# Kernel tuning notes

Hardware: AMD Instinct MI355X
Metric: run time of the kernel (lower is better)

The kernel has to match this reference:

```python
import jax, jax.numpy as jnp
import numpy as np

N_HEAD = 16
N_EMBD = 2048
B, S = 2, 2048


def setup_inputs() -> dict:
    key = jax.random.key(0)
    k1, k2, k3 = jax.random.split(key, 3)
    scale = 0.02
    return {
        "hidden_states": jax.random.normal(k1, (B, S, N_EMBD), dtype=jnp.float32),
        "attention_mask": jnp.ones((B, S), dtype=jnp.float32),
        "w_attn": jax.random.normal(k2, (N_EMBD, 3 * N_EMBD), dtype=jnp.float32) * scale,
        "b_attn": jnp.zeros((3 * N_EMBD,), dtype=jnp.float32),
        "w_proj": jax.random.normal(k3, (N_EMBD, N_EMBD), dtype=jnp.float32) * scale,
        "b_proj": jnp.zeros((N_EMBD,), dtype=jnp.float32),
    }


def reference(hidden_states, attention_mask, w_attn, b_attn, w_proj, b_proj):
    b, s, d = hidden_states.shape
    h = N_HEAD
    dh = d // h
    qkv = hidden_states @ w_attn + b_attn          # [b, s, 3d]
    q, k, v = jnp.split(qkv, 3, axis=-1)
    # [b, s, d] -> [b, h, s, dh]
    q = q.reshape(b, s, h, dh).transpose(0, 2, 1, 3)
    k = k.reshape(b, s, h, dh).transpose(0, 2, 1, 3)
    v = v.reshape(b, s, h, dh).transpose(0, 2, 1, 3)
    scores = jnp.einsum("bhqd,bhkd->bhqk", q, k) / jnp.sqrt(jnp.float32(dh))
    # padding mask: [b, s] -> additive bias [b, 1, 1, s]
    bias = (1.0 - attention_mask)[:, None, None, :] * -10000.0
    attn = jax.nn.softmax(scores + bias, axis=-1)   # dropout p=0 (eval)
    out = jnp.einsum("bhqk,bhkd->bhqd", attn, v)    # [b, h, s, dh]
    out = out.transpose(0, 2, 1, 3).reshape(b, s, d)
    return out @ w_proj + b_proj
```

## Files before the change

kernel.cpp:

```cpp
#include <hip/hip_runtime.h>
#include <stdint.h>

#define B_   2
#define S_   2048
#define D_   2048
#define NH_  16
#define DH_  128
#define N3_  6144

typedef unsigned short u16;
typedef __bf16 bf16x8 __attribute__((ext_vector_type(8)));
typedef float  f32x4  __attribute__((ext_vector_type(4)));

#define QSCALE   (0.08838834764831845f * 1.4426950408889634f)
#define BIASF    (-10000.0f * 1.4426950408889634f)

__device__ __forceinline__ u16 f2bf(float f) {
  union { float f; unsigned u; } v; v.f = f;
  unsigned u = v.u;
  return (u16)((u + 0x7FFFu + ((u >> 16) & 1u)) >> 16);
}

__device__ __forceinline__ float fast_exp2(float x) {
  float r;
  asm("v_exp_f32 %0, %1" : "=v"(r) : "v"(x));
  return r;
}

#define GL2LDS(gsrc, ldst)                                                              \
  __builtin_amdgcn_global_load_lds((const __attribute__((address_space(1))) void*)(gsrc), \
      (__attribute__((address_space(3))) void*)(ldst), 16, 0, 0)

__device__ __forceinline__ int swz_id() {
  int id = blockIdx.y * gridDim.x + blockIdx.x;
  int cpx = (gridDim.x * gridDim.y) >> 3;
  return (id & 7) * cpx + (id >> 3);
}

__global__ void cvt_kernel(const float* __restrict__ in, u16* __restrict__ out, int n4) {
  int i = blockIdx.x * blockDim.x + threadIdx.x;
  int stride = gridDim.x * blockDim.x;
  for (; i < n4; i += stride) {
    float4 v = ((const float4*)in)[i];
    ushort4 o;
    o.x = f2bf(v.x); o.y = f2bf(v.y); o.z = f2bf(v.z); o.w = f2bf(v.w);
    ((ushort4*)out)[i] = o;
  }
}

__global__ void transpose_kernel(const float* __restrict__ in, u16* __restrict__ out,
                                 int K, int N) {
  __shared__ float tile[32][33];
  int tx = threadIdx.x, ty = threadIdx.y;
  int nx = blockIdx.x * 32, ky = blockIdx.y * 32;
#pragma unroll
  for (int j = 0; j < 32; j += 8)
    tile[ty + j][tx] = in[(size_t)(ky + ty + j) * N + nx + tx];
  __syncthreads();
#pragma unroll
  for (int j = 0; j < 32; j += 8)
    out[(size_t)(nx + ty + j) * K + ky + tx] = f2bf(tile[tx][ty + j]);
}


#define KS_ABASE(c, h) (lds + (c) * 24576 + (h) * 8192)
#define KS_BBASE(c, h) (lds + (c) * 24576 + 16384 + (h) * 4096)
#define VMCNT(n) asm volatile("s_waitcnt vmcnt(" #n ")" ::: "memory")
#define LGKM0                                            \
  do {                                                   \
    asm volatile("s_waitcnt lgkmcnt(0)" ::: "memory");   \
    __builtin_amdgcn_sched_barrier(0);                   \
  } while (0)
#define BAR __builtin_amdgcn_s_barrier()

__device__ __forceinline__ void ks_read_set(const u16* __restrict__ Ab,
                                            const u16* __restrict__ Bb,
                                            int wrB, int wcB, int lr, int g,
                                            bf16x8 (&af)[4], bf16x8 (&bf)[4]) {
#pragma unroll
  for (int i = 0; i < 4; ++i) {
    int r = wrB + i * 16 + lr;
    int pr = r >> 1;
    int slot = (((r & 1) << 2) | g) ^ (pr & 7);
    af[i] = *reinterpret_cast<const bf16x8*>(Ab + pr * 64 + slot * 8);
  }
#pragma unroll
  for (int j = 0; j < 4; ++j) {
    int n = wcB + j * 16 + lr;
    int pn = n >> 1;
    int slot = (((n & 1) << 2) | g) ^ (pn & 7);
    bf[j] = *reinterpret_cast<const bf16x8*>(Bb + pn * 64 + slot * 8);
  }
}

__device__ __forceinline__ void ks_mfma(const bf16x8 (&af)[4], const bf16x8 (&bf)[4],
                                        f32x4 (&acc)[4][4]) {
  __builtin_amdgcn_s_setprio(1);
#pragma unroll
  for (int i = 0; i < 4; ++i)
#pragma unroll
    for (int j = 0; j < 4; ++j)
      acc[i][j] = __builtin_amdgcn_mfma_f32_16x16x32_bf16(af[i], bf[j], acc[i][j], 0, 0, 0);
  __builtin_amdgcn_s_setprio(0);
}

template <int KD>
__device__ __forceinline__ void ks_stage(const u16* __restrict__ A,
                                         const u16* __restrict__ BT, u16* lds,
                                         int c, int h, int Tg, int m0, int n0, int t) {
#pragma unroll
  for (int inst = 0; inst < 2; ++inst) {
    int idx = inst * 512 + t;
    int pr = idx >> 3, s = idx & 7, v = s ^ (pr & 7);
    int r = pr * 2 + (v >> 2), g = v & 3;
    GL2LDS(A + (size_t)(m0 + r) * KD + Tg * 64 + h * 32 + g * 8,
           KS_ABASE(c, h) + idx * 8);
  }
  {
    int idx = t;
    int pn = idx >> 3, s = idx & 7, v = s ^ (pn & 7);
    int n = pn * 2 + (v >> 2), g = v & 3;
    GL2LDS(BT + (size_t)(n0 + n) * KD + Tg * 64 + h * 32 + g * 8,
           KS_BBASE(c, h) + idx * 8);
  }
}

template <int KD>
__device__ __forceinline__ void gemm_ks_core(const u16* __restrict__ A,
                                             const u16* __restrict__ BT,
                                             int m0, int n0, u16* lds, f32x4 (&acc)[4][4]) {
  const int NT = KD / 64;
  int t = threadIdx.x, wv = t >> 6, lane = t & 63;
  int g = lane >> 4, lr = lane & 15;
  int wrB = (wv >> 1) * 64, wcB = (wv & 1) * 64;
  bf16x8 af0[4], bf0[4], af1[4], bf1[4];

  ks_stage<KD>(A, BT, lds, 0, 0, 0, m0, n0, t);
  ks_stage<KD>(A, BT, lds, 0, 1, 0, m0, n0, t);
  ks_stage<KD>(A, BT, lds, 1, 0, 1, m0, n0, t);
  ks_stage<KD>(A, BT, lds, 1, 1, 1, m0, n0, t);
  VMCNT(6);
  BAR;
  ks_read_set(KS_ABASE(0, 0), KS_BBASE(0, 0), wrB, wcB, lr, g, af0, bf0);
  LGKM0;
  BAR;

  for (int T = 0; T < NT; ++T) {
    int c = T & 1;
    ks_read_set(KS_ABASE(c, 1), KS_BBASE(c, 1), wrB, wcB, lr, g, af1, bf1);
    if (T + 2 < NT) ks_stage<KD>(A, BT, lds, c, 0, T + 2, m0, n0, t);
    BAR;
    LGKM0;
    ks_mfma(af0, bf0, acc);
    BAR;
    if (T + 2 < NT) {
      VMCNT(3);
      ks_stage<KD>(A, BT, lds, c, 1, T + 2, m0, n0, t);
    } else {
      VMCNT(0);
    }
    BAR;
    if (T + 1 < NT)
      ks_read_set(KS_ABASE(c ^ 1, 0), KS_BBASE(c ^ 1, 0), wrB, wcB, lr, g, af0, bf0);
    LGKM0;
    ks_mfma(af1, bf1, acc);
    BAR;
  }
}

__global__ __launch_bounds__(512, 2) void gemm_qkv_kernel(
    const u16* __restrict__ A, const u16* __restrict__ BT, const float* __restrict__ bias,
    u16* __restrict__ Qb, u16* __restrict__ Kb, u16* __restrict__ VTb) {
  __shared__ __attribute__((aligned(16))) u16 lds[49152];
  f32x4 acc[4][4] = {};
  int sw = swz_id();
  int n0 = (sw % gridDim.x) * 128, m0 = (sw / gridDim.x) * 256;
  gemm_ks_core<2048>(A, BT, m0, n0, lds, acc);
  int t = threadIdx.x, lane = t & 63, wv = t >> 6;
  int g = lane >> 4, lr = lane & 15;
  int wrB = (wv >> 1) * 64, wcB = (wv & 1) * 64;
#pragma unroll
  for (int mi = 0; mi < 4; ++mi) {
    int rowbase = m0 + wrB + mi * 16 + g * 4;
    int b = rowbase >> 11, s = rowbase & 2047;
#pragma unroll
    for (int nj = 0; nj < 4; ++nj) {
      int col = n0 + wcB + nj * 16 + lr;
      float bv = bias[col];
      int sec = col >> 11;
      int within = col & 2047;
      int h = within >> 7, d = within & 127;
      if (sec < 2) {
        float mult = (sec == 0) ? QSCALE : 1.0f;
        u16* dst = (sec == 0 ? Qb : Kb) + ((size_t)(b * NH_ + h) * S_ + s) * DH_ + d;
#pragma unroll
        for (int r = 0; r < 4; ++r) dst[(size_t)r * DH_] = f2bf((acc[mi][nj][r] + bv) * mult);
      } else {
        u16* dst = VTb + ((size_t)(b * NH_ + h) * DH_ + d) * S_ + s;
        ushort4 pk;
        pk.x = f2bf(acc[mi][nj][0] + bv); pk.y = f2bf(acc[mi][nj][1] + bv);
        pk.z = f2bf(acc[mi][nj][2] + bv); pk.w = f2bf(acc[mi][nj][3] + bv);
        *reinterpret_cast<ushort4*>(dst) = pk;
      }
    }
  }
}

__global__ __launch_bounds__(512, 2) void gemm_proj_kernel(
    const u16* __restrict__ A, const u16* __restrict__ BT, const float* __restrict__ bias,
    float* __restrict__ out) {
  __shared__ __attribute__((aligned(16))) u16 lds[49152];
  f32x4 acc[4][4] = {};
  int sw = swz_id();
  int n0 = (sw % gridDim.x) * 128, m0 = (sw / gridDim.x) * 256;
  gemm_ks_core<2048>(A, BT, m0, n0, lds, acc);
  int t = threadIdx.x, lane = t & 63, wv = t >> 6;
  int g = lane >> 4, lr = lane & 15;
  int wrB = (wv >> 1) * 64, wcB = (wv & 1) * 64;
#pragma unroll
  for (int mi = 0; mi < 4; ++mi) {
    int rowbase = m0 + wrB + mi * 16 + g * 4;
#pragma unroll
    for (int nj = 0; nj < 4; ++nj) {
      int col = n0 + wcB + nj * 16 + lr;
      float bv = bias[col];
      float* dst = out + (size_t)rowbase * D_ + col;
#pragma unroll
      for (int r = 0; r < 4; ++r) dst[(size_t)r * D_] = acc[mi][nj][r] + bv;
    }
  }
}

__global__ __launch_bounds__(256) void attn_kernel(
    const u16* __restrict__ Qb, const u16* __restrict__ Kb, const u16* __restrict__ VTb,
    const float* __restrict__ mask, u16* __restrict__ AO) {
  __shared__ __attribute__((aligned(16))) u16 Ks[2][64 * 128];
  __shared__ __attribute__((aligned(16))) u16 Vs[2][128 * 64];
  __shared__ __attribute__((aligned(16))) u16 Ps[4][16 * 64];
  __shared__ float bias_lds[S_];

  int t = threadIdx.x, w = t >> 6, lane = t & 63;
  int g = lane >> 4, lr = lane & 15;
  int sw = swz_id();
  int qt = sw & 31, bh = sw >> 5;
  int b = bh >> 4;
  const u16* Qh = Qb + (size_t)bh * S_ * DH_;
  const u16* Kh = Kb + (size_t)bh * S_ * DH_;
  const u16* Vh = VTb + (size_t)bh * DH_ * S_;
  int q0 = qt * 64 + w * 16;

  for (int i = t; i < S_; i += 256)
    bias_lds[i] = (1.0f - mask[b * S_ + i]) * BIASF;

  bf16x8 aq[4];
#pragma unroll
  for (int kk = 0; kk < 4; ++kk)
    aq[kk] = *reinterpret_cast<const bf16x8*>(Qh + (size_t)(q0 + lr) * DH_ + kk * 32 + g * 8);

  f32x4 oacc[8] = {};
  float m_r[4], l_r[4];
#pragma unroll
  for (int r = 0; r < 4; ++r) { m_r[r] = -1e30f; l_r[r] = 0.f; }

  __syncthreads();

#define STAGE_KV(buf, s0base)                                                    \
  {                                                                              \
    _Pragma("unroll")                                                            \
    for (int i = 0; i < 4; ++i) {                                                \
      int idx = i * 256 + t;                                                     \
      int row = idx >> 4, slot = idx & 15;                                       \
      GL2LDS(Kh + (size_t)((s0base) + row) * DH_ + ((slot ^ (row & 7)) * 8),     \
             &Ks[buf][idx * 8]);                                                 \
    }                                                                            \
    _Pragma("unroll")                                                            \
    for (int i = 0; i < 4; ++i) {                                                \
      int idx = i * 256 + t;                                                     \
      int row = idx >> 3, slot = idx & 7;                                        \
      GL2LDS(Vh + (size_t)row * S_ + (s0base) + ((slot ^ (row & 7)) * 8),        \
             &Vs[buf][idx * 8]);                                                 \
    }                                                                            \
  }

  STAGE_KV(0, 0);
  const int NT = S_ / 64;
  for (int it = 0; it < NT; ++it) {
    int cur = it & 1;
    if (it + 1 < NT) {
      STAGE_KV(cur ^ 1, (it + 1) * 64);
      asm volatile("s_waitcnt vmcnt(8)" ::: "memory");
    } else {
      asm volatile("s_waitcnt vmcnt(0)" ::: "memory");
    }
    __builtin_amdgcn_s_barrier();
    __builtin_amdgcn_sched_barrier(0);

    f32x4 sacc[4] = {};
#pragma unroll
    for (int kk = 0; kk < 4; ++kk) {
#pragma unroll
      for (int n = 0; n < 4; ++n) {
        int c = lr + 16 * n;
        bf16x8 bk = *reinterpret_cast<const bf16x8*>(
            &Ks[cur][c * 128 + ((((kk << 2) | g) ^ (c & 7)) * 8)]);
        sacc[n] = __builtin_amdgcn_mfma_f32_16x16x32_bf16(aq[kk], bk, sacc[n], 0, 0, 0);
      }
    }

    int s0 = it * 64;
    float sv[4][4], mx[4];
#pragma unroll
    for (int r = 0; r < 4; ++r) {
#pragma unroll
      for (int n = 0; n < 4; ++n) sv[r][n] = sacc[n][r] + bias_lds[s0 + lr + 16 * n];
      float m2 = fmaxf(fmaxf(sv[r][0], sv[r][1]), fmaxf(sv[r][2], sv[r][3]));
#pragma unroll
      for (int off = 1; off < 16; off <<= 1) m2 = fmaxf(m2, __shfl_xor(m2, off));
      mx[r] = m2;
    }
    float gmax = fmaxf(fmaxf(mx[0] - m_r[0], mx[1] - m_r[1]),
                       fmaxf(mx[2] - m_r[2], mx[3] - m_r[3]));
    if (__any(gmax > 8.f)) {
#pragma unroll
      for (int r = 0; r < 4; ++r) {
        float mnew = fmaxf(m_r[r], mx[r]);
        float f = fast_exp2(m_r[r] - mnew);
        m_r[r] = mnew;
        l_r[r] *= f;
#pragma unroll
        for (int no = 0; no < 8; ++no) oacc[no][r] *= f;
      }
    }
#pragma unroll
    for (int r = 0; r < 4; ++r) {
      int prow = g * 4 + r;
#pragma unroll
      for (int n = 0; n < 4; ++n) {
        float p = fast_exp2(sv[r][n] - m_r[r]);
        l_r[r] += p;
        int col = lr + 16 * n;
        Ps[w][prow * 64 + ((((col >> 3) ^ (prow & 7)) << 3) + (col & 7))] = f2bf(p);
      }
    }

#pragma unroll
    for (int kk2 = 0; kk2 < 2; ++kk2) {
      bf16x8 ap = *reinterpret_cast<const bf16x8*>(
          &Ps[w][lr * 64 + ((((kk2 << 2) | g) ^ (lr & 7)) * 8)]);
#pragma unroll
      for (int no = 0; no < 8; ++no) {
        int d = lr + 16 * no;
        bf16x8 bv = *reinterpret_cast<const bf16x8*>(
            &Vs[cur][d * 64 + ((((kk2 << 2) | g) ^ (d & 7)) * 8)]);
        oacc[no] = __builtin_amdgcn_mfma_f32_16x16x32_bf16(ap, bv, oacc[no], 0, 0, 0);
      }
    }
    __builtin_amdgcn_sched_barrier(0);
    __builtin_amdgcn_s_barrier();
  }
#undef STAGE_KV

#pragma unroll
  for (int r = 0; r < 4; ++r) {
    float s = l_r[r];
#pragma unroll
    for (int off = 1; off < 16; off <<= 1) s += __shfl_xor(s, off);
    float inv = 1.0f / s;
    int qrow = q0 + g * 4 + r;
    int h = bh & 15;
    u16* dst = AO + ((size_t)(b * S_ + qrow)) * D_ + h * DH_;
#pragma unroll
    for (int no = 0; no < 8; ++no) dst[lr + 16 * no] = f2bf(oacc[no][r] * inv);
  }
}

extern "C" void kernel_launch(void* const* d_in, const int* in_sizes, int n_in,
                              void* d_out, int out_size, void* d_ws, size_t ws_size,
                              hipStream_t stream) {
  const float* h_in   = (const float*)d_in[0];
  const float* mask   = (const float*)d_in[1];
  const float* w_attn = (const float*)d_in[2];
  const float* b_attn = (const float*)d_in[3];
  const float* w_proj = (const float*)d_in[4];
  const float* b_proj = (const float*)d_in[5];
  float* out = (float*)d_out;

  char* ws = (char*)d_ws;
  u16* Hb  = (u16*)(ws);
  u16* W1T = (u16*)(ws + 16777216);
  u16* W2T = (u16*)(ws + 41943040);
  u16* Qb  = (u16*)(ws + 50331648);
  u16* Kb  = (u16*)(ws + 67108864);
  u16* VTb = (u16*)(ws + 83886080);
  u16* AO  = Hb;

  cvt_kernel<<<2048, 256, 0, stream>>>(h_in, Hb, (B_ * S_ * D_) / 4);
  dim3 tb(32, 8);
  transpose_kernel<<<dim3(N3_ / 32, D_ / 32), tb, 0, stream>>>(w_attn, W1T, D_, N3_);
  transpose_kernel<<<dim3(D_ / 32, D_ / 32), tb, 0, stream>>>(w_proj, W2T, D_, D_);
  gemm_qkv_kernel<<<dim3(N3_ / 128, (B_ * S_) / 256), 512, 0, stream>>>(
      Hb, W1T, b_attn, Qb, Kb, VTb);
  attn_kernel<<<dim3(S_ / 64, B_ * NH_), 256, 0, stream>>>(Qb, Kb, VTb, mask, AO);
  gemm_proj_kernel<<<dim3(D_ / 128, (B_ * S_) / 256), 512, 0, stream>>>(AO, W2T, b_proj, out);
}
```

Baseline: 445.3 us.

## Transpose attention MFMAs to keep P in registers and drop LDS round-trip

Swaps the operand order of the QK^T and PV MFMAs so each lane holds one query row's scores. Softmax statistics then need only two cross-lane shuffles, and P is packed with v_cvt_pk_bf16 and redistributed via shuffles instead of being written to and re-read from LDS. The change also adds s_setprio around the MFMA blocks, vectorizes the output and bias accesses, and relaxes the GEMM launch bounds to one block per SIMD. It trades LDS traffic and barriers for extra shuffles and selects, and the GEMM register budget change could alter occupancy.

```diff
diff --git a/kernel.cpp b/kernel.cpp
--- a/kernel.cpp
+++ b/kernel.cpp
@@ -24,6 +24,12 @@
 __device__ __forceinline__ float fast_exp2(float x) {
   float r;
   asm("v_exp_f32 %0, %1" : "=v"(r) : "v"(x));
+  return r;
+}
+
+__device__ __forceinline__ unsigned cvtpk(float lo, float hi) {
+  unsigned r;
+  asm("v_cvt_pk_bf16_f32 %0, %1, %2" : "=v"(r) : "v"(lo), "v"(hi));
   return r;
 }
 
@@ -168,7 +174,7 @@
   }
 }
 
-__global__ __launch_bounds__(512, 2) void gemm_qkv_kernel(
+__global__ __launch_bounds__(512, 1) void gemm_qkv_kernel(
     const u16* __restrict__ A, const u16* __restrict__ BT, const float* __restrict__ bias,
     u16* __restrict__ Qb, u16* __restrict__ Kb, u16* __restrict__ VTb) {
   __shared__ __attribute__((aligned(16))) u16 lds[49152];
@@ -206,7 +212,7 @@
   }
 }
 
-__global__ __launch_bounds__(512, 2) void gemm_proj_kernel(
+__global__ __launch_bounds__(512, 1) void gemm_proj_kernel(
     const u16* __restrict__ A, const u16* __restrict__ BT, const float* __restrict__ bias,
     float* __restrict__ out) {
   __shared__ __attribute__((aligned(16))) u16 lds[49152];
@@ -236,7 +242,6 @@
     const float* __restrict__ mask, u16* __restrict__ AO) {
   __shared__ __attribute__((aligned(16))) u16 Ks[2][64 * 128];
   __shared__ __attribute__((aligned(16))) u16 Vs[2][128 * 64];
-  __shared__ __attribute__((aligned(16))) u16 Ps[4][16 * 64];
   __shared__ float bias_lds[S_];
 
   int t = threadIdx.x, w = t >> 6, lane = t & 63;
@@ -252,15 +257,13 @@
   for (int i = t; i < S_; i += 256)
     bias_lds[i] = (1.0f - mask[b * S_ + i]) * BIASF;
 
-  bf16x8 aq[4];
+  bf16x8 bq[4];
 #pragma unroll
   for (int kk = 0; kk < 4; ++kk)
-    aq[kk] = *reinterpret_cast<const bf16x8*>(Qh + (size_t)(q0 + lr) * DH_ + kk * 32 + g * 8);
+    bq[kk] = *reinterpret_cast<const bf16x8*>(Qh + (size_t)(q0 + lr) * DH_ + kk * 32 + g * 8);
 
   f32x4 oacc[8] = {};
-  float m_r[4], l_r[4];
-#pragma unroll
-  for (int r = 0; r < 4; ++r) { m_r[r] = -1e30f; l_r[r] = 0.f; }
+  float m_r = -1e30f, l_r = 0.f;
 
   __syncthreads();
 
@@ -296,81 +299,91 @@
     __builtin_amdgcn_sched_barrier(0);
 
     f32x4 sacc[4] = {};
+    __builtin_amdgcn_s_setprio(1);
 #pragma unroll
     for (int kk = 0; kk < 4; ++kk) {
 #pragma unroll
       for (int n = 0; n < 4; ++n) {
-        int c = lr + 16 * n;
-        bf16x8 bk = *reinterpret_cast<const bf16x8*>(
-            &Ks[cur][c * 128 + ((((kk << 2) | g) ^ (c & 7)) * 8)]);
-        sacc[n] = __builtin_amdgcn_mfma_f32_16x16x32_bf16(aq[kk], bk, sacc[n], 0, 0, 0);
+        int row = lr + 16 * n;
+        bf16x8 ak = *reinterpret_cast<const bf16x8*>(
+            &Ks[cur][row * 128 + ((((kk << 2) | g) ^ (row & 7)) * 8)]);
+        sacc[n] = __builtin_amdgcn_mfma_f32_16x16x32_bf16(ak, bq[kk], sacc[n], 0, 0, 0);
       }
     }
+    __builtin_amdgcn_s_setprio(0);
 
     int s0 = it * 64;
-    float sv[4][4], mx[4];
-#pragma unroll
-    for (int r = 0; r < 4; ++r) {
-#pragma unroll
-      for (int n = 0; n < 4; ++n) sv[r][n] = sacc[n][r] + bias_lds[s0 + lr + 16 * n];
-      float m2 = fmaxf(fmaxf(sv[r][0], sv[r][1]), fmaxf(sv[r][2], sv[r][3]));
-#pragma unroll
-      for (int off = 1; off < 16; off <<= 1) m2 = fmaxf(m2, __shfl_xor(m2, off));
-      mx[r] = m2;
-    }
-    float gmax = fmaxf(fmaxf(mx[0] - m_r[0], mx[1] - m_r[1]),
-                       fmaxf(mx[2] - m_r[2], mx[3] - m_r[3]));
-    if (__any(gmax > 8.f)) {
-#pragma unroll
-      for (int r = 0; r < 4; ++r) {
-        float mnew = fmaxf(m_r[r], mx[r]);
-        float f = fast_exp2(m_r[r] - mnew);
-        m_r[r] = mnew;
-        l_r[r] *= f;
-#pragma unroll
-        for (int no = 0; no < 8; ++no) oacc[no][r] *= f;
-      }
-    }
-#pragma unroll
-    for (int r = 0; r < 4; ++r) {
-      int prow = g * 4 + r;
-#pragma unroll
-      for (int n = 0; n < 4; ++n) {
-        float p = fast_exp2(sv[r][n] - m_r[r]);
-        l_r[r] += p;
-        int col = lr + 16 * n;
-        Ps[w][prow * 64 + ((((col >> 3) ^ (prow & 7)) << 3) + (col & 7))] = f2bf(p);
-      }
-    }
-
+    float sv[4][4];
+    float mloc = -3e38f;
+#pragma unroll
+    for (int n = 0; n < 4; ++n) {
+      float4 bb = *reinterpret_cast<const float4*>(&bias_lds[s0 + 16 * n + g * 4]);
+      sv[n][0] = sacc[n][0] + bb.x; sv[n][1] = sacc[n][1] + bb.y;
+      sv[n][2] = sacc[n][2] + bb.z; sv[n][3] = sacc[n][3] + bb.w;
+      mloc = fmaxf(mloc, fmaxf(fmaxf(sv[n][0], sv[n][1]), fmaxf(sv[n][2], sv[n][3])));
+    }
+    float mx = fmaxf(mloc, __shfl_xor(mloc, 16));
+    mx = fmaxf(mx, __shfl_xor(mx, 32));
+
+    if (__any(mx - m_r > 8.f)) {
+      float mnew = fmaxf(m_r, mx);
+      float f = fast_exp2(m_r - mnew);
+      m_r = mnew;
+      l_r *= f;
+#pragma unroll
+      for (int no = 0; no < 8; ++no) oacc[no] *= f;
+    }
+
+    unsigned pku[4][2];
+#pragma unroll
+    for (int n = 0; n < 4; ++n) {
+      float p0 = fast_exp2(sv[n][0] - m_r), p1 = fast_exp2(sv[n][1] - m_r);
+      float p2 = fast_exp2(sv[n][2] - m_r), p3 = fast_exp2(sv[n][3] - m_r);
+      l_r += (p0 + p1) + (p2 + p3);
+      pku[n][0] = cvtpk(p0, p1);
+      pku[n][1] = cvtpk(p2, p3);
+    }
+
+    int srcA = ((g & 1) << 5) + lr;
+    int srcB = srcA + 16;
+    bool hi = (g >> 1) != 0;
 #pragma unroll
     for (int kk2 = 0; kk2 < 2; ++kk2) {
-      bf16x8 ap = *reinterpret_cast<const bf16x8*>(
-          &Ps[w][lr * 64 + ((((kk2 << 2) | g) ^ (lr & 7)) * 8)]);
+      unsigned a0 = __shfl(pku[2 * kk2][0], srcA), a1 = __shfl(pku[2 * kk2 + 1][0], srcA);
+      unsigned b0 = __shfl(pku[2 * kk2][1], srcA), b1 = __shfl(pku[2 * kk2 + 1][1], srcA);
+      unsigned c0 = __shfl(pku[2 * kk2][0], srcB), c1 = __shfl(pku[2 * kk2 + 1][0], srcB);
+      unsigned d0 = __shfl(pku[2 * kk2][1], srcB), d1 = __shfl(pku[2 * kk2 + 1][1], srcB);
+      union { uint4 u; bf16x8 v; } pa;
+      pa.u.x = hi ? a1 : a0; pa.u.y = hi ? b1 : b0;
+      pa.u.z = hi ? c1 : c0; pa.u.w = hi ? d1 : d0;
+      __builtin_amdgcn_s_setprio(1);
 #pragma unroll
       for (int no = 0; no < 8; ++no) {
         int d = lr + 16 * no;
-        bf16x8 bv = *reinterpret_cast<const bf16x8*>(
+        bf16x8 av = *reinterpret_cast<const bf16x8*>(
             &Vs[cur][d * 64 + ((((kk2 << 2) | g) ^ (d & 7)) * 8)]);
-        oacc[no] = __builtin_amdgcn_mfma_f32_16x16x32_bf16(ap, bv, oacc[no], 0, 0, 0);
+        oacc[no] = __builtin_amdgcn_mfma_f32_16x16x32_bf16(av, pa.v, oacc[no], 0, 0, 0);
       }
+      __builtin_amdgcn_s_setprio(0);
     }
     __builtin_amdgcn_sched_barrier(0);
     __builtin_amdgcn_s_barrier();
   }
 #undef STAGE_KV
 
-#pragma unroll
-  for (int r = 0; r < 4; ++r) {
-    float s = l_r[r];
-#pragma unroll
-    for (int off = 1; off < 16; off <<= 1) s += __shfl_xor(s, off);
-    float inv = 1.0f / s;
-    int qrow = q0 + g * 4 + r;
-    int h = bh & 15;
-    u16* dst = AO + ((size_t)(b * S_ + qrow)) * D_ + h * DH_;
-#pragma unroll
-    for (int no = 0; no < 8; ++no) dst[lr + 16 * no] = f2bf(oacc[no][r] * inv);
+  float s = l_r;
+  s += __shfl_xor(s, 16);
+  s += __shfl_xor(s, 32);
+  float inv = 1.0f / s;
+  int h = bh & 15;
+  int q = q0 + lr;
+  u16* dst = AO + ((size_t)(b * S_ + q)) * D_ + h * DH_ + g * 4;
+#pragma unroll
+  for (int no = 0; no < 8; ++no) {
+    ushort4 pk4;
+    pk4.x = f2bf(oacc[no][0] * inv); pk4.y = f2bf(oacc[no][1] * inv);
+    pk4.z = f2bf(oacc[no][2] * inv); pk4.w = f2bf(oacc[no][3] * inv);
+    *reinterpret_cast<ushort4*>(dst + 16 * no) = pk4;
   }
 }
 
```

After: 434.7 us. -2.4%, faster.
